# Performance work log

Hardware: AMD Instinct MI355X
Metric: run time of the kernel (lower is better)

The kernel has to match this reference:

```python
import jax, jax.numpy as jnp
import numpy as np

B, N, F, H, R = 16, 64, 64, 4, 50
C = F * H  # n_coefficients = n_heads * hidden_features
CUTOFF = 5.0  # ExpNormalSmearing cutoff_upper (cutoff_lower = 0)


def _dense(k, fin, fout):
    s = 1.0 / np.sqrt(fin)
    return jax.random.uniform(k, (fin, fout), jnp.float32, -s, s)


def setup_inputs() -> dict:
    key = jax.random.key(0)
    ks = jax.random.split(key, 20)
    start = float(np.exp(-CUTOFF))
    return {
        "h": jax.random.normal(ks[0], (B, N, F), jnp.float32),
        "x": jax.random.normal(ks[1], (B, N, 3), jnp.float32),
        "v": jax.random.normal(ks[2], (B, N, 3), jnp.float32) * 0.1,
        # edge model (ContinuousFilterConvolutionWithConcatenation)
        "W_in": _dense(ks[3], 2 * F, R), "b_in": jnp.zeros((R,), jnp.float32),
        "rbf_means": jnp.linspace(start, 1.0, R).astype(jnp.float32),
        "rbf_betas": jnp.full((R,), (2.0 / R * (1.0 - start)) ** -2, jnp.float32),
        "W_e1": _dense(ks[4], 2 * F + R + 1, F), "b_e1": jnp.zeros((F,), jnp.float32),
        "W_e2": _dense(ks[5], F, F), "b_e2": jnp.zeros((F,), jnp.float32),
        # semantic attention
        "W_sem": _dense(ks[6], F, H), "b_sem": jnp.zeros((H,), jnp.float32),
        "log_gamma": -jnp.log(jnp.linspace(1.0, 5.0, H)).astype(jnp.float32),
        # spatial attention
        "W_xmix": _dense(ks[7], C, C),
        "W_post1": _dense(ks[8], C, F), "b_post1": jnp.zeros((F,), jnp.float32),
        "W_post2": _dense(ks[9], F, F), "b_post2": jnp.zeros((F,), jnp.float32),
        # node update
        "W_node1": _dense(ks[10], F + C + F, F), "b_node1": jnp.zeros((F,), jnp.float32),
        "W_node2": _dense(ks[11], F, F), "b_node2": jnp.zeros((F,), jnp.float32),
        # velocity update
        "W_vel1": _dense(ks[12], F, F), "b_vel1": jnp.zeros((F,), jnp.float32),
        "W_vel2": _dense(ks[13], F, 1),
        "W_vmix": _dense(ks[14], C, 1),
    }


def reference(h, x, v, W_in, b_in, rbf_means, rbf_betas, W_e1, b_e1, W_e2, b_e2,
              W_sem, b_sem, log_gamma, W_xmix, W_post1, b_post1, W_post2, b_post2,
              W_node1, b_node1, W_node2, b_node2, W_vel1, b_vel1, W_vel2, W_vmix):
    silu = jax.nn.silu
    n = h.shape[-2]
    # pairwise displacement x_j - x_i : (B, N, N, 3)
    x_minus_xt = x[..., None, :, :] - x[..., :, None, :]
    d = jnp.sqrt(jax.nn.relu((x_minus_xt ** 2).sum(-1, keepdims=True)) + 1e-5)  # (B,N,N,1)
    # pairwise node features [h_j, h_i] : (B, N, N, 2F)
    hj = jnp.broadcast_to(h[..., None, :, :], h.shape[:-2] + (n, n, h.shape[-1]))
    hi = jnp.broadcast_to(h[..., :, None, :], hj.shape)
    h_cat = jnp.concatenate([hj, hi], -1)
    # edge model: RBF-smeared continuous-filter conv with concatenation
    h_mid = h_cat @ W_in + b_in  # (B,N,N,R)
    cut = 0.5 * (jnp.cos(d * (jnp.pi / CUTOFF)) + 1.0) * (d < CUTOFF)
    rbf = cut * jnp.exp(-rbf_betas * (jnp.exp(-d) - rbf_means) ** 2)  # (B,N,N,R)
    h_e = jnp.concatenate([h_cat, rbf * h_mid, d], -1)
    h_e = silu(h_e @ W_e1 + b_e1) @ W_e2 + b_e2  # (B,N,N,F)
    # attentions, softmax over neighbor axis (-2), diagonal masked out
    eye = jnp.eye(n, dtype=h.dtype)[:, :, None]
    sem = jax.nn.celu(h_e @ W_sem + b_sem, alpha=2.0) - 1e5 * eye
    sem = jax.nn.softmax(sem, axis=-2)  # (B,N,N,H)
    euc = jax.nn.softmax(-(d + 1e5 * eye) * jnp.exp(log_gamma), axis=-2)  # (B,N,N,H)
    att = euc * sem
    att = att / att.sum(-2, keepdims=True)
    # per-head attention-weighted edge features, flattened (F outer, H inner)
    h_e_att = (h_e[..., :, None] * att[..., None, :]).reshape(att.shape[:-1] + (F * H,))
    # spatial attention on unit displacement vectors
    coeff = jnp.tanh(h_e_att @ W_xmix)  # (B,N,N,C)
    x_hat = x_minus_xt / (d + 1e-5)
    comb = x_hat[..., None, :] * coeff[..., None]  # (B,N,N,C,3)
    comb_sum = comb.mean(axis=-3)  # mean over neighbors -> (B,N,C,3)
    h_comb = (comb_sum ** 2).sum(-1)  # invariant squared norms (B,N,C)
    h_comb = silu(silu(h_comb @ W_post1 + b_post1) @ W_post2 + b_post2)
    # node update (residual)
    h_agg = h_e_att.sum(axis=-2)  # (B,N,C)
    h_out = h + silu(silu(jnp.concatenate([h, h_agg, h_comb], -1) @ W_node1 + b_node1) @ W_node2 + b_node2)
    # equivariant velocity / coordinate update
    delta_v = jnp.einsum('...ijcd,c->...id', comb, W_vmix[:, 0]) / n  # v_mixing + mean over j
    gate = 2.0 * jax.nn.sigmoid(silu(h_out @ W_vel1 + b_vel1) @ W_vel2)  # double_sigmoid, (B,N,1)
    v_out = delta_v + gate * v
    x_out = x + v_out
    return h_out, x_out, v_out
```

## Files before the change

kernel.cpp:

```cpp
#include <hip/hip_runtime.h>
#include <math.h>

#define NB 16
#define NN 64
#define NF 64
#define NH 4
#define NR 50
#define NC 256

typedef __attribute__((ext_vector_type(8))) short short8;
typedef __attribute__((ext_vector_type(4))) float f32x4;

#define WS_WE1 0
#define WS_WE2 (1536 * 8)
#define WS_WX  (2048 * 8)
#define MID_F  40960
#define HAGG_F 172032
#define COMB_F 434176

__device__ __forceinline__ float siluf(float x) { return x / (1.f + __expf(-x)); }
__device__ __forceinline__ float tanhfast(float x) { return 1.f - 2.f / (__expf(2.f * x) + 1.f); }

__device__ __forceinline__ ushort f2bf(float f) {
    union { float f; unsigned u; } v; v.f = f;
    unsigned u = v.u;
    return (ushort)((u + 0x7FFFu + ((u >> 16) & 1u)) >> 16);
}
__device__ __forceinline__ float bf1(ushort u) {
    union { unsigned u; float f; } c; c.u = ((unsigned)u) << 16; return c.f;
}
__device__ __forceinline__ float bflo(unsigned u) {
    union { unsigned u; float f; } c; c.u = u << 16; return c.f;
}
__device__ __forceinline__ float bfhi(unsigned u) {
    union { unsigned u; float f; } c; c.u = u & 0xFFFF0000u; return c.f;
}

__device__ __forceinline__ float wave_max(float v) {
#pragma unroll
    for (int s = 32; s >= 1; s >>= 1) v = fmaxf(v, __shfl_xor(v, s));
    return v;
}
__device__ __forceinline__ float wave_sum(float v) {
#pragma unroll
    for (int s = 32; s >= 1; s >>= 1) v += __shfl_xor(v, s);
    return v;
}

__global__ __launch_bounds__(256)
void prep_kernel(const float* __restrict__ W_e1, const float* __restrict__ W_e2,
                 const float* __restrict__ W_xmix,
                 const float* __restrict__ h, const float* __restrict__ W_in,
                 const float* __restrict__ b_in,
                 short* __restrict__ wpack, float* __restrict__ mid)
{
    int blk = blockIdx.x, t = threadIdx.x;
    if (blk < 40) {
        int s = blk * 256 + t;
        short8 val;
        if (s < 1536) {
            int cl = s & 15, g = (s >> 4) & 3, q = s >> 6;
            int ks = q % 6, nt = q / 6;
            int c = nt * 16 + cl, k0 = 32 * ks + 8 * g;
#pragma unroll
            for (int i = 0; i < 8; i++) {
                int k = k0 + i;
                float f = (k < 179) ? W_e1[k * NF + c] : 0.f;
                val[i] = (short)f2bf(f);
            }
            *(short8*)(&wpack[WS_WE1 + s * 8]) = val;
        } else if (s < 2048) {
            int u = s - 1536;
            int cl = u & 15, g = (u >> 4) & 3, q = u >> 6;
            int ks = q & 1, nt = q >> 1;
            int c = nt * 16 + cl, k0 = 32 * ks + 8 * g;
#pragma unroll
            for (int i = 0; i < 8; i++) val[i] = (short)f2bf(W_e2[(k0 + i) * NF + c]);
            *(short8*)(&wpack[WS_WE2 + u * 8]) = val;
        } else {
            int u = s - 2048;
            int cl = u & 15, g = (u >> 4) & 3, q = u >> 6;
            int ks = q & 7, wn = q >> 3;
            int c = (wn >> 2) * 64 + (wn & 3) * 16 + cl, k0 = 32 * ks + 8 * g;
#pragma unroll
            for (int i = 0; i < 8; i++) val[i] = (short)f2bf(W_xmix[(k0 + i) * NC + c]);
            *(short8*)(&wpack[WS_WX + u * 8]) = val;
        }
    } else {
        int idx = (blk - 40) * 256 + t;
        int node = idx >> 7, rr = idx & 127;
        const float* hn = h + node * NF;
        if (rr < 50) {
            float acc = 0.f;
#pragma unroll 8
            for (int k = 0; k < 64; k++) acc += hn[k] * W_in[k * NR + rr];
            mid[node * 128 + rr] = acc;
        } else if (rr >= 64 && rr < 114) {
            int r = rr - 64;
            float acc = b_in[r];
#pragma unroll 8
            for (int k = 0; k < 64; k++) acc += hn[k] * W_in[(64 + k) * NR + r];
            mid[node * 128 + rr] = acc;
        }
    }
}

__global__ __launch_bounds__(256)
void sake_edge_kernel(
    const float* __restrict__ h, const float* __restrict__ x,
    const float* __restrict__ mid,
    const float* __restrict__ rbf_means, const float* __restrict__ rbf_betas,
    const float* __restrict__ b_e1, const float* __restrict__ b_e2,
    const float* __restrict__ W_sem, const float* __restrict__ b_sem,
    const float* __restrict__ log_gamma,
    const short* __restrict__ wpack,
    float* __restrict__ hagg_g, float* __restrict__ comb_g)
{
    const int bi = blockIdx.x;
    const int b  = bi >> 6;
    const int i  = bi & 63;
    const int t  = threadIdx.x;
    const int w  = t >> 6, l = t & 63, lr = l & 15, lg = l >> 4;

    __shared__ __align__(16) short s_A[24 * 64 * 8];
    __shared__ short s_he[64 * 66];
    __shared__ float s_comb[768];
    __shared__ float s_xhat[256];
    __shared__ float s_att[256];
    __shared__ float s_wsem[256];
    __shared__ float s_midi[52];

    const short8* A8  = (const short8*)s_A;
    short8*       A8w = (short8*)s_A;
    const short8* We1p = (const short8*)(wpack + WS_WE1);
    const short8* We2p = (const short8*)(wpack + WS_WE2);
    const short8* Wxp  = (const short8*)(wpack + WS_WX);

    s_wsem[t] = W_sem[t];
    if (t < 50) s_midi[t] = mid[(b * 64 + i) * 128 + 64 + t];
    if (t < 64) {
        int j = t;
        float dx = x[(b * NN + j) * 3 + 0] - x[(b * NN + i) * 3 + 0];
        float dy = x[(b * NN + j) * 3 + 1] - x[(b * NN + i) * 3 + 1];
        float dz = x[(b * NN + j) * 3 + 2] - x[(b * NN + i) * 3 + 2];
        float d2 = dx * dx + dy * dy + dz * dz;
        float d  = sqrtf(fmaxf(d2, 0.f) + 1e-5f);
        float inv = 1.f / (d + 1e-5f);
        s_xhat[j * 4 + 0] = dx * inv;
        s_xhat[j * 4 + 1] = dy * inv;
        s_xhat[j * 4 + 2] = dz * inv;
        s_xhat[j * 4 + 3] = d;
    }
    __syncthreads();

    {
        int j = t & 63, p = t >> 6;
        const float* hj = h + (b * 64 + j) * NF;
        const float* hi = h + (b * 64 + i) * NF;
#pragma unroll
        for (int q = 0; q < 2; q++) {
            int sl = 2 * p + q;
            short8 vj, vi;
#pragma unroll
            for (int e = 0; e < 8; e++) {
                vj[e] = (short)f2bf(hj[sl * 8 + e]);
                vi[e] = (short)f2bf(hi[sl * 8 + e]);
            }
            A8w[sl * 64 + j] = vj;
            A8w[(8 + sl) * 64 + j] = vi;
        }
        float d = s_xhat[j * 4 + 3];
        float cut = 0.5f * (__cosf(d * 0.6283185307179586f) + 1.f) * (d < 5.f ? 1.f : 0.f);
        float emd = __expf(-d);
        const float* midj = mid + (b * 64 + j) * 128;
#pragma unroll
        for (int q = 0; q < 2; q++) {
            int sl = 16 + 2 * p + q;
            short8 val;
#pragma unroll
            for (int e = 0; e < 8; e++) {
                int r = (sl - 16) * 8 + e;
                float o;
                if (r < 50) {
                    float m = midj[r] + s_midi[r];
                    float df = emd - rbf_means[r];
                    o = cut * __expf(-rbf_betas[r] * df * df) * m;
                } else if (r == 50) o = d;
                else o = 0.f;
                val[e] = (short)f2bf(o);
            }
            A8w[sl * 64 + j] = val;
        }
    }
    __syncthreads();

    {
        f32x4 acc[4];
#pragma unroll
        for (int jt = 0; jt < 4; jt++) { acc[jt][0] = 0.f; acc[jt][1] = 0.f; acc[jt][2] = 0.f; acc[jt][3] = 0.f; }
        for (int ks = 0; ks < 6; ks++) {
            short8 bb = We1p[(w * 6 + ks) * 64 + l];
#pragma unroll
            for (int jt = 0; jt < 4; jt++) {
                short8 aa = A8[(ks * 4 + lg) * 64 + jt * 16 + lr];
                acc[jt] = __builtin_amdgcn_mfma_f32_16x16x32_bf16(aa, bb, acc[jt], 0, 0, 0);
            }
        }
        __syncthreads();
        float be = b_e1[w * 16 + lr];
        int f = w * 16 + lr;
#pragma unroll
        for (int jt = 0; jt < 4; jt++)
#pragma unroll
            for (int r = 0; r < 4; r++) {
                int j = jt * 16 + lg * 4 + r;
                s_A[((f >> 3) * 64 + j) * 8 + (f & 7)] = (short)f2bf(siluf(acc[jt][r] + be));
            }
        __syncthreads();
    }

    {
        f32x4 acc[4];
#pragma unroll
        for (int jt = 0; jt < 4; jt++) { acc[jt][0] = 0.f; acc[jt][1] = 0.f; acc[jt][2] = 0.f; acc[jt][3] = 0.f; }
#pragma unroll
        for (int ks = 0; ks < 2; ks++) {
            short8 bb = We2p[(w * 2 + ks) * 64 + l];
#pragma unroll
            for (int jt = 0; jt < 4; jt++) {
                short8 aa = A8[(ks * 4 + lg) * 64 + jt * 16 + lr];
                acc[jt] = __builtin_amdgcn_mfma_f32_16x16x32_bf16(aa, bb, acc[jt], 0, 0, 0);
            }
        }
        float be2 = b_e2[w * 16 + lr];
        int f = w * 16 + lr;
#pragma unroll
        for (int jt = 0; jt < 4; jt++)
#pragma unroll
            for (int r = 0; r < 4; r++) {
                int j = jt * 16 + lg * 4 + r;
                s_he[j * 66 + f] = (short)f2bf(acc[jt][r] + be2);
            }
        __syncthreads();
    }

    {
        int hh = w, j = l;
        float acc = b_sem[hh];
        const unsigned* hp = (const unsigned*)(s_he + j * 66);
#pragma unroll 8
        for (int q = 0; q < 32; q++) {
            unsigned u = hp[q];
            acc += bflo(u) * s_wsem[(2 * q) * 4 + hh] + bfhi(u) * s_wsem[(2 * q + 1) * 4 + hh];
        }
        float cel = fmaxf(acc, 0.f) + fminf(0.f, 2.f * (__expf(0.5f * acc) - 1.f));
        float diag = (j == i) ? 1e5f : 0.f;
        float slog = cel - diag;
        float m1 = wave_max(slog);
        float e1 = __expf(slog - m1);
        float sem = e1 / wave_sum(e1);
        float gam = __expf(log_gamma[hh]);
        float elog = -(s_xhat[j * 4 + 3] + diag) * gam;
        float m2 = wave_max(elog);
        float e2 = __expf(elog - m2);
        float euc = e2 / wave_sum(e2);
        float a = sem * euc;
        a = a / wave_sum(a);
        s_att[j * 4 + hh] = a;
    }
    __syncthreads();

    {
        int f = t >> 2, hh = t & 3;
        float acc = 0.f;
#pragma unroll 8
        for (int j = 0; j < 64; j++) acc += bf1((ushort)s_he[j * 66 + f]) * s_att[j * 4 + hh];
        hagg_g[bi * 256 + t] = acc;
    }

    f32x4 acc[4][4];
#pragma unroll
    for (int jt = 0; jt < 4; jt++)
#pragma unroll
        for (int nt = 0; nt < 4; nt++) { acc[jt][nt][0] = 0.f; acc[jt][nt][1] = 0.f; acc[jt][nt][2] = 0.f; acc[jt][nt][3] = 0.f; }

    for (int half = 0; half < 2; half++) {
        {
            int j = t & 63, kc = t >> 6;
            float a0 = s_att[j * 4 + 0], a1 = s_att[j * 4 + 1];
            float a2 = s_att[j * 4 + 2], a3 = s_att[j * 4 + 3];
#pragma unroll
            for (int s = 0; s < 4; s++) {
                int sl = kc * 4 + s;
                int kbase = half * 128 + sl * 8;
                unsigned u = *(const unsigned*)(s_he + j * 66 + (kbase >> 2));
                float h0 = bflo(u), h1 = bfhi(u);
                short8 val;
                val[0] = (short)f2bf(h0 * a0); val[1] = (short)f2bf(h0 * a1);
                val[2] = (short)f2bf(h0 * a2); val[3] = (short)f2bf(h0 * a3);
                val[4] = (short)f2bf(h1 * a0); val[5] = (short)f2bf(h1 * a1);
                val[6] = (short)f2bf(h1 * a2); val[7] = (short)f2bf(h1 * a3);
                A8w[sl * 64 + j] = val;
            }
        }
        __syncthreads();
#pragma unroll
        for (int ks = 0; ks < 4; ks++) {
            short8 aa[4], bb[4];
#pragma unroll
            for (int jt = 0; jt < 4; jt++) aa[jt] = A8[(ks * 4 + lg) * 64 + jt * 16 + lr];
#pragma unroll
            for (int nt = 0; nt < 4; nt++) bb[nt] = Wxp[((w * 4 + nt) * 8 + half * 4 + ks) * 64 + l];
#pragma unroll
            for (int jt = 0; jt < 4; jt++)
#pragma unroll
                for (int nt = 0; nt < 4; nt++)
                    acc[jt][nt] = __builtin_amdgcn_mfma_f32_16x16x32_bf16(aa[jt], bb[nt], acc[jt][nt], 0, 0, 0);
        }
        __syncthreads();
    }

    {
#pragma unroll
        for (int nt = 0; nt < 4; nt++) {
            float p0 = 0.f, p1 = 0.f, p2 = 0.f;
#pragma unroll
            for (int jt = 0; jt < 4; jt++)
#pragma unroll
                for (int r = 0; r < 4; r++) {
                    int j = jt * 16 + lg * 4 + r;
                    float th = tanhfast(acc[jt][nt][r]);
                    p0 += s_xhat[j * 4 + 0] * th;
                    p1 += s_xhat[j * 4 + 1] * th;
                    p2 += s_xhat[j * 4 + 2] * th;
                }
            p0 += __shfl_xor(p0, 16); p0 += __shfl_xor(p0, 32);
            p1 += __shfl_xor(p1, 16); p1 += __shfl_xor(p1, 32);
            p2 += __shfl_xor(p2, 16); p2 += __shfl_xor(p2, 32);
            if (lg == 0) {
                int c = w * 64 + nt * 16 + lr;
                s_comb[c * 3 + 0] = p0 * (1.f / 64.f);
                s_comb[c * 3 + 1] = p1 * (1.f / 64.f);
                s_comb[c * 3 + 2] = p2 * (1.f / 64.f);
            }
        }
    }
    __syncthreads();
    {
        float* cg = comb_g + bi * 768;
        cg[t] = s_comb[t];
        cg[256 + t] = s_comb[256 + t];
        cg[512 + t] = s_comb[512 + t];
    }
}

__global__ __launch_bounds__(256)
void sake_tail_kernel(
    const float* __restrict__ h, const float* __restrict__ x, const float* __restrict__ v,
    const float* __restrict__ hagg_g, const float* __restrict__ comb_g,
    const float* __restrict__ W_post1, const float* __restrict__ b_post1,
    const float* __restrict__ W_post2, const float* __restrict__ b_post2,
    const float* __restrict__ W_node1, const float* __restrict__ b_node1,
    const float* __restrict__ W_node2, const float* __restrict__ b_node2,
    const float* __restrict__ W_vel1, const float* __restrict__ b_vel1,
    const float* __restrict__ W_vel2, const float* __restrict__ W_vmix,
    float* __restrict__ out_h, float* __restrict__ out_x, float* __restrict__ out_v)
{
    const int t = threadIdx.x, r = t >> 6, l = t & 63;
    const int node = blockIdx.x * 4 + r;

    __shared__ float s_in[4][384];
    __shared__ float s_hcp[4][256];
    __shared__ float s_p1[4][64];
    __shared__ float s_ho[4][64];

    float cmb[4][3];
#pragma unroll
    for (int q = 0; q < 4; q++) {
        int c = q * 64 + l;
        float c0 = comb_g[node * 768 + c * 3 + 0];
        float c1 = comb_g[node * 768 + c * 3 + 1];
        float c2 = comb_g[node * 768 + c * 3 + 2];
        cmb[q][0] = c0; cmb[q][1] = c1; cmb[q][2] = c2;
        s_hcp[r][c] = c0 * c0 + c1 * c1 + c2 * c2;
    }
    float hi = h[node * NF + l];
    s_in[r][l] = hi;
#pragma unroll
    for (int q = 0; q < 4; q++) s_in[r][64 + q * 64 + l] = hagg_g[node * 256 + q * 64 + l];
    __syncthreads();

    float a1 = b_post1[l];
#pragma unroll 8
    for (int c = 0; c < 256; c++) a1 += s_hcp[r][c] * W_post1[c * NF + l];
    s_p1[r][l] = siluf(a1);
    __syncthreads();

    float a2 = b_post2[l];
#pragma unroll 8
    for (int k = 0; k < 64; k++) a2 += s_p1[r][k] * W_post2[k * NF + l];
    s_in[r][320 + l] = siluf(a2);
    __syncthreads();

    float a3 = b_node1[l];
#pragma unroll 8
    for (int k = 0; k < 384; k++) a3 += s_in[r][k] * W_node1[k * NF + l];
    s_p1[r][l] = siluf(a3);
    __syncthreads();

    float a4 = b_node2[l];
#pragma unroll 8
    for (int k = 0; k < 64; k++) a4 += s_p1[r][k] * W_node2[k * NF + l];
    float ho = hi + siluf(a4);
    out_h[node * NF + l] = ho;
    s_ho[r][l] = ho;
    __syncthreads();

    float a5 = b_vel1[l];
#pragma unroll 8
    for (int k = 0; k < 64; k++) a5 += s_ho[r][k] * W_vel1[k * NF + l];
    float g = wave_sum(siluf(a5) * W_vel2[l]);
    g = 2.f / (1.f + __expf(-g));

    float dv[3];
#pragma unroll
    for (int k = 0; k < 3; k++) {
        float p = 0.f;
#pragma unroll
        for (int q = 0; q < 4; q++) p += cmb[q][k] * W_vmix[q * 64 + l];
        dv[k] = wave_sum(p);
    }
    if (l < 3) {
        float vout = dv[l] + g * v[node * 3 + l];
        out_v[node * 3 + l] = vout;
        out_x[node * 3 + l] = x[node * 3 + l] + vout;
    }
}

extern "C" void kernel_launch(void* const* d_in, const int* in_sizes, int n_in,
                              void* d_out, int out_size, void* d_ws, size_t ws_size,
                              hipStream_t stream) {
    const float* h        = (const float*)d_in[0];
    const float* x        = (const float*)d_in[1];
    const float* v        = (const float*)d_in[2];
    const float* W_in     = (const float*)d_in[3];
    const float* b_in     = (const float*)d_in[4];
    const float* rbf_m    = (const float*)d_in[5];
    const float* rbf_b    = (const float*)d_in[6];
    const float* W_e1     = (const float*)d_in[7];
    const float* b_e1     = (const float*)d_in[8];
    const float* W_e2     = (const float*)d_in[9];
    const float* b_e2     = (const float*)d_in[10];
    const float* W_sem    = (const float*)d_in[11];
    const float* b_sem    = (const float*)d_in[12];
    const float* log_g    = (const float*)d_in[13];
    const float* W_xmix   = (const float*)d_in[14];
    const float* W_post1  = (const float*)d_in[15];
    const float* b_post1  = (const float*)d_in[16];
    const float* W_post2  = (const float*)d_in[17];
    const float* b_post2  = (const float*)d_in[18];
    const float* W_node1  = (const float*)d_in[19];
    const float* b_node1  = (const float*)d_in[20];
    const float* W_node2  = (const float*)d_in[21];
    const float* b_node2  = (const float*)d_in[22];
    const float* W_vel1   = (const float*)d_in[23];
    const float* b_vel1   = (const float*)d_in[24];
    const float* W_vel2   = (const float*)d_in[25];
    const float* W_vmix   = (const float*)d_in[26];

    float* out   = (float*)d_out;
    float* out_h = out;
    float* out_x = out + NB * NN * NF;
    float* out_v = out + NB * NN * NF + NB * NN * 3;

    short* wpack = (short*)d_ws;
    float* wsf   = (float*)d_ws;
    float* mid   = wsf + MID_F;
    float* hagg  = wsf + HAGG_F;
    float* comb  = wsf + COMB_F;

    prep_kernel<<<552, 256, 0, stream>>>(W_e1, W_e2, W_xmix, h, W_in, b_in, wpack, mid);

    sake_edge_kernel<<<NB * NN, 256, 0, stream>>>(
        h, x, mid, rbf_m, rbf_b, b_e1, b_e2, W_sem, b_sem, log_g,
        wpack, hagg, comb);

    sake_tail_kernel<<<256, 256, 0, stream>>>(
        h, x, v, hagg, comb,
        W_post1, b_post1, W_post2, b_post2, W_node1, b_node1, W_node2, b_node2,
        W_vel1, b_vel1, W_vel2, W_vmix, out_h, out_x, out_v);
}
```

Before: 64.41 us.

## Precompute per-node W_e1 projections and shrink edge MFMA K; split tail per node

The h_j and h_i parts of the first edge MLP layer are now projected once per node in the prep kernel (with bias folded in) and added as accumulator initial values. The edge kernel's bf16 MFMA then covers only the 51 RBF/distance columns, so K drops from 192 to 64 and the h staging into shared memory goes away. The tail kernel moves to one node per block, with the K dimension of each small matvec split across four waves and reduced through shared memory. Bf16 conversion switches to the native cast, and comb results are written straight to global. In exchange, the edge kernel reads fp32 e1 rows from global for every (j,f), and more tail blocks are launched.

```diff
diff --git a/kernel.cpp b/kernel.cpp
--- a/kernel.cpp
+++ b/kernel.cpp
@@ -11,20 +11,20 @@
 typedef __attribute__((ext_vector_type(8))) short short8;
 typedef __attribute__((ext_vector_type(4))) float f32x4;
 
-#define WS_WE1 0
-#define WS_WE2 (1536 * 8)
-#define WS_WX  (2048 * 8)
-#define MID_F  40960
-#define HAGG_F 172032
-#define COMB_F 434176
+#define WS_WE1R 0
+#define WS_WE2  4096
+#define WS_WX   8192
+#define MID_F   36864
+#define E1_F    (MID_F + 131072)
+#define HAGG_F  (E1_F + 131072)
+#define COMB_F  (HAGG_F + 262144)
 
 __device__ __forceinline__ float siluf(float x) { return x / (1.f + __expf(-x)); }
 __device__ __forceinline__ float tanhfast(float x) { return 1.f - 2.f / (__expf(2.f * x) + 1.f); }
 
-__device__ __forceinline__ ushort f2bf(float f) {
-    union { float f; unsigned u; } v; v.f = f;
-    unsigned u = v.u;
-    return (ushort)((u + 0x7FFFu + ((u >> 16) & 1u)) >> 16);
+__device__ __forceinline__ short f2bfs(float f) {
+    __bf16 b = (__bf16)f;
+    union { __bf16 b; short s; } u; u.b = b; return u.s;
 }
 __device__ __forceinline__ float bf1(ushort u) {
     union { unsigned u; float f; } c; c.u = ((unsigned)u) << 16; return c.f;
@@ -48,69 +48,82 @@
 }
 
 __global__ __launch_bounds__(256)
-void prep_kernel(const float* __restrict__ W_e1, const float* __restrict__ W_e2,
-                 const float* __restrict__ W_xmix,
+void prep_kernel(const float* __restrict__ W_e1, const float* __restrict__ b_e1,
+                 const float* __restrict__ W_e2, const float* __restrict__ W_xmix,
                  const float* __restrict__ h, const float* __restrict__ W_in,
                  const float* __restrict__ b_in,
-                 short* __restrict__ wpack, float* __restrict__ mid)
+                 short* __restrict__ wpack, float* __restrict__ mid, float* __restrict__ e1)
 {
     int blk = blockIdx.x, t = threadIdx.x;
-    if (blk < 40) {
+    if (blk < 36) {
         int s = blk * 256 + t;
         short8 val;
-        if (s < 1536) {
+        if (s < 512) {
             int cl = s & 15, g = (s >> 4) & 3, q = s >> 6;
-            int ks = q % 6, nt = q / 6;
+            int ks = q & 1, nt = q >> 1;
             int c = nt * 16 + cl, k0 = 32 * ks + 8 * g;
 #pragma unroll
             for (int i = 0; i < 8; i++) {
-                int k = k0 + i;
-                float f = (k < 179) ? W_e1[k * NF + c] : 0.f;
-                val[i] = (short)f2bf(f);
-            }
-            *(short8*)(&wpack[WS_WE1 + s * 8]) = val;
-        } else if (s < 2048) {
-            int u = s - 1536;
+                int kr = k0 + i;
+                float f = (kr < 50) ? W_e1[(128 + kr) * NF + c] : (kr == 50 ? W_e1[178 * NF + c] : 0.f);
+                val[i] = f2bfs(f);
+            }
+            *(short8*)(&wpack[WS_WE1R + s * 8]) = val;
+        } else if (s < 1024) {
+            int u = s - 512;
             int cl = u & 15, g = (u >> 4) & 3, q = u >> 6;
             int ks = q & 1, nt = q >> 1;
             int c = nt * 16 + cl, k0 = 32 * ks + 8 * g;
 #pragma unroll
-            for (int i = 0; i < 8; i++) val[i] = (short)f2bf(W_e2[(k0 + i) * NF + c]);
+            for (int i = 0; i < 8; i++) val[i] = f2bfs(W_e2[(k0 + i) * NF + c]);
             *(short8*)(&wpack[WS_WE2 + u * 8]) = val;
         } else {
-            int u = s - 2048;
+            int u = s - 1024;
             int cl = u & 15, g = (u >> 4) & 3, q = u >> 6;
             int ks = q & 7, wn = q >> 3;
             int c = (wn >> 2) * 64 + (wn & 3) * 16 + cl, k0 = 32 * ks + 8 * g;
 #pragma unroll
-            for (int i = 0; i < 8; i++) val[i] = (short)f2bf(W_xmix[(k0 + i) * NC + c]);
+            for (int i = 0; i < 8; i++) val[i] = f2bfs(W_xmix[(k0 + i) * NC + c]);
             *(short8*)(&wpack[WS_WX + u * 8]) = val;
         }
     } else {
-        int idx = (blk - 40) * 256 + t;
-        int node = idx >> 7, rr = idx & 127;
-        const float* hn = h + node * NF;
-        if (rr < 50) {
+        int node = blk - 36;
+        __shared__ float s_hn[64];
+        if (t < 64) s_hn[t] = h[node * NF + t];
+        __syncthreads();
+        if (t < 64) {
             float acc = 0.f;
 #pragma unroll 8
-            for (int k = 0; k < 64; k++) acc += hn[k] * W_in[k * NR + rr];
-            mid[node * 128 + rr] = acc;
-        } else if (rr >= 64 && rr < 114) {
-            int r = rr - 64;
+            for (int k = 0; k < 64; k++) acc += s_hn[k] * W_e1[k * NF + t];
+            e1[node * 128 + t] = acc;
+        } else if (t < 128) {
+            int f = t - 64;
+            float acc = b_e1[f];
+#pragma unroll 8
+            for (int k = 0; k < 64; k++) acc += s_hn[k] * W_e1[(64 + k) * NF + f];
+            e1[node * 128 + 64 + f] = acc;
+        } else if (t < 178) {
+            int r = t - 128;
+            float acc = 0.f;
+#pragma unroll 8
+            for (int k = 0; k < 64; k++) acc += s_hn[k] * W_in[k * NR + r];
+            mid[node * 128 + r] = acc;
+        } else if (t >= 192 && t < 242) {
+            int r = t - 192;
             float acc = b_in[r];
 #pragma unroll 8
-            for (int k = 0; k < 64; k++) acc += hn[k] * W_in[(64 + k) * NR + r];
-            mid[node * 128 + rr] = acc;
+            for (int k = 0; k < 64; k++) acc += s_hn[k] * W_in[(64 + k) * NR + r];
+            mid[node * 128 + 64 + r] = acc;
         }
     }
 }
 
 __global__ __launch_bounds__(256)
 void sake_edge_kernel(
-    const float* __restrict__ h, const float* __restrict__ x,
-    const float* __restrict__ mid,
+    const float* __restrict__ x,
+    const float* __restrict__ mid, const float* __restrict__ e1,
     const float* __restrict__ rbf_means, const float* __restrict__ rbf_betas,
-    const float* __restrict__ b_e1, const float* __restrict__ b_e2,
+    const float* __restrict__ b_e2,
     const float* __restrict__ W_sem, const float* __restrict__ b_sem,
     const float* __restrict__ log_gamma,
     const short* __restrict__ wpack,
@@ -122,9 +135,8 @@
     const int t  = threadIdx.x;
     const int w  = t >> 6, l = t & 63, lr = l & 15, lg = l >> 4;
 
-    __shared__ __align__(16) short s_A[24 * 64 * 8];
+    __shared__ __align__(16) short s_A[16 * 64 * 8];
     __shared__ short s_he[64 * 66];
-    __shared__ float s_comb[768];
     __shared__ float s_xhat[256];
     __shared__ float s_att[256];
     __shared__ float s_wsem[256];
@@ -132,7 +144,7 @@
 
     const short8* A8  = (const short8*)s_A;
     short8*       A8w = (short8*)s_A;
-    const short8* We1p = (const short8*)(wpack + WS_WE1);
+    const short8* We1p = (const short8*)(wpack + WS_WE1R);
     const short8* We2p = (const short8*)(wpack + WS_WE2);
     const short8* Wxp  = (const short8*)(wpack + WS_WX);
 
@@ -155,31 +167,17 @@
 
     {
         int j = t & 63, p = t >> 6;
-        const float* hj = h + (b * 64 + j) * NF;
-        const float* hi = h + (b * 64 + i) * NF;
-#pragma unroll
-        for (int q = 0; q < 2; q++) {
-            int sl = 2 * p + q;
-            short8 vj, vi;
-#pragma unroll
-            for (int e = 0; e < 8; e++) {
-                vj[e] = (short)f2bf(hj[sl * 8 + e]);
-                vi[e] = (short)f2bf(hi[sl * 8 + e]);
-            }
-            A8w[sl * 64 + j] = vj;
-            A8w[(8 + sl) * 64 + j] = vi;
-        }
         float d = s_xhat[j * 4 + 3];
         float cut = 0.5f * (__cosf(d * 0.6283185307179586f) + 1.f) * (d < 5.f ? 1.f : 0.f);
         float emd = __expf(-d);
         const float* midj = mid + (b * 64 + j) * 128;
 #pragma unroll
         for (int q = 0; q < 2; q++) {
-            int sl = 16 + 2 * p + q;
+            int sl = 2 * p + q;
             short8 val;
 #pragma unroll
             for (int e = 0; e < 8; e++) {
-                int r = (sl - 16) * 8 + e;
+                int r = sl * 8 + e;
                 float o;
                 if (r < 50) {
                     float m = midj[r] + s_midi[r];
@@ -187,7 +185,7 @@
                     o = cut * __expf(-rbf_betas[r] * df * df) * m;
                 } else if (r == 50) o = d;
                 else o = 0.f;
-                val[e] = (short)f2bf(o);
+                val[e] = f2bfs(o);
             }
             A8w[sl * 64 + j] = val;
         }
@@ -195,11 +193,20 @@
     __syncthreads();
 
     {
+        int f = w * 16 + lr;
+        const float* e1b = e1 + (size_t)b * 64 * 128;
+        float e1i_v = e1b[i * 128 + 64 + f];
         f32x4 acc[4];
 #pragma unroll
-        for (int jt = 0; jt < 4; jt++) { acc[jt][0] = 0.f; acc[jt][1] = 0.f; acc[jt][2] = 0.f; acc[jt][3] = 0.f; }
-        for (int ks = 0; ks < 6; ks++) {
-            short8 bb = We1p[(w * 6 + ks) * 64 + l];
+        for (int jt = 0; jt < 4; jt++)
+#pragma unroll
+            for (int r = 0; r < 4; r++) {
+                int j = jt * 16 + lg * 4 + r;
+                acc[jt][r] = e1b[j * 128 + f] + e1i_v;
+            }
+#pragma unroll
+        for (int ks = 0; ks < 2; ks++) {
+            short8 bb = We1p[(w * 2 + ks) * 64 + l];
 #pragma unroll
             for (int jt = 0; jt < 4; jt++) {
                 short8 aa = A8[(ks * 4 + lg) * 64 + jt * 16 + lr];
@@ -207,14 +214,12 @@
             }
         }
         __syncthreads();
-        float be = b_e1[w * 16 + lr];
-        int f = w * 16 + lr;
 #pragma unroll
         for (int jt = 0; jt < 4; jt++)
 #pragma unroll
             for (int r = 0; r < 4; r++) {
                 int j = jt * 16 + lg * 4 + r;
-                s_A[((f >> 3) * 64 + j) * 8 + (f & 7)] = (short)f2bf(siluf(acc[jt][r] + be));
+                s_A[((f >> 3) * 64 + j) * 8 + (f & 7)] = f2bfs(siluf(acc[jt][r]));
             }
         __syncthreads();
     }
@@ -239,7 +244,7 @@
 #pragma unroll
             for (int r = 0; r < 4; r++) {
                 int j = jt * 16 + lg * 4 + r;
-                s_he[j * 66 + f] = (short)f2bf(acc[jt][r] + be2);
+                s_he[j * 66 + f] = f2bfs(acc[jt][r] + be2);
             }
         __syncthreads();
     }
@@ -257,8 +262,8 @@
         float diag = (j == i) ? 1e5f : 0.f;
         float slog = cel - diag;
         float m1 = wave_max(slog);
-        float e1 = __expf(slog - m1);
-        float sem = e1 / wave_sum(e1);
+        float e1v = __expf(slog - m1);
+        float sem = e1v / wave_sum(e1v);
         float gam = __expf(log_gamma[hh]);
         float elog = -(s_xhat[j * 4 + 3] + diag) * gam;
         float m2 = wave_max(elog);
@@ -296,10 +301,10 @@
                 unsigned u = *(const unsigned*)(s_he + j * 66 + (kbase >> 2));
                 float h0 = bflo(u), h1 = bfhi(u);
                 short8 val;
-                val[0] = (short)f2bf(h0 * a0); val[1] = (short)f2bf(h0 * a1);
-                val[2] = (short)f2bf(h0 * a2); val[3] = (short)f2bf(h0 * a3);
-                val[4] = (short)f2bf(h1 * a0); val[5] = (short)f2bf(h1 * a1);
-                val[6] = (short)f2bf(h1 * a2); val[7] = (short)f2bf(h1 * a3);
+                val[0] = f2bfs(h0 * a0); val[1] = f2bfs(h0 * a1);
+                val[2] = f2bfs(h0 * a2); val[3] = f2bfs(h0 * a3);
+                val[4] = f2bfs(h1 * a0); val[5] = f2bfs(h1 * a1);
+                val[6] = f2bfs(h1 * a2); val[7] = f2bfs(h1 * a3);
                 A8w[sl * 64 + j] = val;
             }
         }
@@ -339,18 +344,12 @@
             p2 += __shfl_xor(p2, 16); p2 += __shfl_xor(p2, 32);
             if (lg == 0) {
                 int c = w * 64 + nt * 16 + lr;
-                s_comb[c * 3 + 0] = p0 * (1.f / 64.f);
-                s_comb[c * 3 + 1] = p1 * (1.f / 64.f);
-                s_comb[c * 3 + 2] = p2 * (1.f / 64.f);
-            }
-        }
-    }
-    __syncthreads();
-    {
-        float* cg = comb_g + bi * 768;
-        cg[t] = s_comb[t];
-        cg[256 + t] = s_comb[256 + t];
-        cg[512 + t] = s_comb[512 + t];
+                float* cg = comb_g + bi * 768 + c * 3;
+                cg[0] = p0 * (1.f / 64.f);
+                cg[1] = p1 * (1.f / 64.f);
+                cg[2] = p2 * (1.f / 64.f);
+            }
+        }
     }
 }
 
@@ -366,74 +365,102 @@
     const float* __restrict__ W_vel2, const float* __restrict__ W_vmix,
     float* __restrict__ out_h, float* __restrict__ out_x, float* __restrict__ out_v)
 {
-    const int t = threadIdx.x, r = t >> 6, l = t & 63;
-    const int node = blockIdx.x * 4 + r;
-
-    __shared__ float s_in[4][384];
-    __shared__ float s_hcp[4][256];
-    __shared__ float s_p1[4][64];
-    __shared__ float s_ho[4][64];
-
-    float cmb[4][3];
-#pragma unroll
-    for (int q = 0; q < 4; q++) {
-        int c = q * 64 + l;
-        float c0 = comb_g[node * 768 + c * 3 + 0];
-        float c1 = comb_g[node * 768 + c * 3 + 1];
-        float c2 = comb_g[node * 768 + c * 3 + 2];
-        cmb[q][0] = c0; cmb[q][1] = c1; cmb[q][2] = c2;
-        s_hcp[r][c] = c0 * c0 + c1 * c1 + c2 * c2;
-    }
-    float hi = h[node * NF + l];
-    s_in[r][l] = hi;
-#pragma unroll
-    for (int q = 0; q < 4; q++) s_in[r][64 + q * 64 + l] = hagg_g[node * 256 + q * 64 + l];
-    __syncthreads();
-
-    float a1 = b_post1[l];
-#pragma unroll 8
-    for (int c = 0; c < 256; c++) a1 += s_hcp[r][c] * W_post1[c * NF + l];
-    s_p1[r][l] = siluf(a1);
-    __syncthreads();
-
-    float a2 = b_post2[l];
-#pragma unroll 8
-    for (int k = 0; k < 64; k++) a2 += s_p1[r][k] * W_post2[k * NF + l];
-    s_in[r][320 + l] = siluf(a2);
-    __syncthreads();
-
-    float a3 = b_node1[l];
-#pragma unroll 8
-    for (int k = 0; k < 384; k++) a3 += s_in[r][k] * W_node1[k * NF + l];
-    s_p1[r][l] = siluf(a3);
-    __syncthreads();
-
-    float a4 = b_node2[l];
-#pragma unroll 8
-    for (int k = 0; k < 64; k++) a4 += s_p1[r][k] * W_node2[k * NF + l];
-    float ho = hi + siluf(a4);
-    out_h[node * NF + l] = ho;
-    s_ho[r][l] = ho;
-    __syncthreads();
-
-    float a5 = b_vel1[l];
-#pragma unroll 8
-    for (int k = 0; k < 64; k++) a5 += s_ho[r][k] * W_vel1[k * NF + l];
-    float g = wave_sum(siluf(a5) * W_vel2[l]);
-    g = 2.f / (1.f + __expf(-g));
-
-    float dv[3];
-#pragma unroll
-    for (int k = 0; k < 3; k++) {
+    const int node = blockIdx.x;
+    const int t = threadIdx.x, w = t >> 6, l = t & 63;
+
+    __shared__ float s_in[384];
+    __shared__ float s_hcp[256];
+    __shared__ float s_cmb[3][256];
+    __shared__ float s_red[4][64];
+    __shared__ float s_vec[64];
+    __shared__ float s_ho[64];
+
+    {
+        const float* cg = comb_g + node * 768;
+        float c0 = cg[t * 3 + 0], c1 = cg[t * 3 + 1], c2 = cg[t * 3 + 2];
+        s_cmb[0][t] = c0; s_cmb[1][t] = c1; s_cmb[2][t] = c2;
+        s_hcp[t] = c0 * c0 + c1 * c1 + c2 * c2;
+        if (t < 64) s_in[t] = h[node * NF + t];
+        s_in[64 + t] = hagg_g[node * 256 + t];
+    }
+    __syncthreads();
+
+    {
         float p = 0.f;
-#pragma unroll
-        for (int q = 0; q < 4; q++) p += cmb[q][k] * W_vmix[q * 64 + l];
-        dv[k] = wave_sum(p);
-    }
-    if (l < 3) {
-        float vout = dv[l] + g * v[node * 3 + l];
-        out_v[node * 3 + l] = vout;
-        out_x[node * 3 + l] = x[node * 3 + l] + vout;
+#pragma unroll 8
+        for (int k = w * 64; k < w * 64 + 64; k++) p += s_hcp[k] * W_post1[k * NF + l];
+        s_red[w][l] = p;
+    }
+    __syncthreads();
+    {
+        float a = b_post1[l] + s_red[0][l] + s_red[1][l] + s_red[2][l] + s_red[3][l];
+        if (w == 0) s_vec[l] = siluf(a);
+    }
+    __syncthreads();
+
+    {
+        float p = 0.f;
+#pragma unroll
+        for (int k = w * 16; k < w * 16 + 16; k++) p += s_vec[k] * W_post2[k * NF + l];
+        s_red[w][l] = p;
+    }
+    __syncthreads();
+    {
+        float a = b_post2[l] + s_red[0][l] + s_red[1][l] + s_red[2][l] + s_red[3][l];
+        if (w == 0) s_in[320 + l] = siluf(a);
+    }
+    __syncthreads();
+
+    {
+        float p = 0.f;
+#pragma unroll 8
+        for (int k = w * 96; k < w * 96 + 96; k++) p += s_in[k] * W_node1[k * NF + l];
+        s_red[w][l] = p;
+    }
+    __syncthreads();
+    {
+        float a = b_node1[l] + s_red[0][l] + s_red[1][l] + s_red[2][l] + s_red[3][l];
+        if (w == 0) s_vec[l] = siluf(a);
+    }
+    __syncthreads();
+
+    {
+        float p = 0.f;
+#pragma unroll
+        for (int k = w * 16; k < w * 16 + 16; k++) p += s_vec[k] * W_node2[k * NF + l];
+        s_red[w][l] = p;
+    }
+    __syncthreads();
+    {
+        float a = b_node2[l] + s_red[0][l] + s_red[1][l] + s_red[2][l] + s_red[3][l];
+        float ho = s_in[l] + siluf(a);
+        if (w == 0) { out_h[node * NF + l] = ho; s_ho[l] = ho; }
+    }
+    __syncthreads();
+
+    {
+        float p = 0.f;
+#pragma unroll
+        for (int k = w * 16; k < w * 16 + 16; k++) p += s_ho[k] * W_vel1[k * NF + l];
+        s_red[w][l] = p;
+    }
+    __syncthreads();
+    {
+        float a = b_vel1[l] + s_red[0][l] + s_red[1][l] + s_red[2][l] + s_red[3][l];
+        float v1 = siluf(a);
+        float g = wave_sum(v1 * W_vel2[l]);
+        g = 2.f / (1.f + __expf(-g));
+        if (w < 3) {
+            float pv = 0.f;
+#pragma unroll
+            for (int q = 0; q < 4; q++) pv += s_cmb[w][q * 64 + l] * W_vmix[q * 64 + l];
+            float dv = wave_sum(pv);
+            if (l == 0) {
+                float vout = dv + g * v[node * 3 + w];
+                out_v[node * 3 + w] = vout;
+                out_x[node * 3 + w] = x[node * 3 + w] + vout;
+            }
+        }
     }
 }
 
@@ -476,16 +503,18 @@
     short* wpack = (short*)d_ws;
     float* wsf   = (float*)d_ws;
     float* mid   = wsf + MID_F;
+    float* e1    = wsf + E1_F;
     float* hagg  = wsf + HAGG_F;
     float* comb  = wsf + COMB_F;
 
-    prep_kernel<<<552, 256, 0, stream>>>(W_e1, W_e2, W_xmix, h, W_in, b_in, wpack, mid);
+    prep_kernel<<<36 + 1024, 256, 0, stream>>>(W_e1, b_e1, W_e2, W_xmix, h, W_in, b_in,
+                                               wpack, mid, e1);
 
     sake_edge_kernel<<<NB * NN, 256, 0, stream>>>(
-        h, x, mid, rbf_m, rbf_b, b_e1, b_e2, W_sem, b_sem, log_g,
+        x, mid, e1, rbf_m, rbf_b, b_e2, W_sem, b_sem, log_g,
         wpack, hagg, comb);
 
-    sake_tail_kernel<<<256, 256, 0, stream>>>(
+    sake_tail_kernel<<<1024, 256, 0, stream>>>(
         h, x, v, hagg, comb,
         W_post1, b_post1, W_post2, b_post2, W_node1, b_node1, W_node2, b_node2,
         W_vel1, b_vel1, W_vel2, W_vmix, out_h, out_x, out_v);
```

Result: faster. 56.05 us (-13.0%).
